# Kernel optimization log

Hardware: AMD Instinct MI355X
Metric: run time of the kernel (lower is better)

The kernel has to match this reference:

```python
import jax, jax.numpy as jnp
import numpy as np

B, IN, OUT = 8192, 256, 256

def setup_inputs() -> dict:
    key = jax.random.key(0)
    k1, k2 = jax.random.split(key)
    x = jax.random.normal(k1, (B, IN), dtype=jnp.float32)
    # kaiming_uniform_(a=sqrt(5)) -> U(-bound, bound), bound = sqrt(6/((1+a^2)*fan_in)) = sqrt(1/fan_in)
    bound = 1.0 / np.sqrt(IN + 1)
    weight = jax.random.uniform(k2, (OUT, IN + 1), dtype=jnp.float32, minval=-bound, maxval=bound)
    return {"x": x, "weight": weight}

def reference(x, weight):
    # augment x with ones column (bias term): (B, IN+1)
    x_aug = jnp.concatenate([x, jnp.ones((x.shape[0], 1), dtype=x.dtype)], axis=1)
    # lrelu(x, k) = clamp(k * x, min=0) = relu(weight * x) broadcast over (B, OUT, IN+1)
    y = jnp.maximum(weight[None, :, :] * x_aug[:, None, :], 0.0)
    return jnp.sum(y, axis=2)  # (B, OUT)
```

## Files before the change

### kernel.cpp

```cpp
#include <hip/hip_runtime.h>
#include <hip/hip_bf16.h>
#include <cstdint>


typedef short short8 __attribute__((ext_vector_type(8)));
typedef float f32x4 __attribute__((ext_vector_type(4)));

#define IN_F 256
#define OUT_F 256
#define KC 512
#define BM 32
#define BN 64
#define BK 64
#define NSTEP (KC / BK)

static __device__ __forceinline__ short f2bf(float f) {
    return __builtin_bit_cast(short, static_cast<__bf16>(f));
}

__global__ __launch_bounds__(64) void prep_kernel(const float* __restrict__ w,
                                                  short* __restrict__ Wcat,
                                                  float* __restrict__ bias) {
    const int o = blockIdx.x;
    const int t = threadIdx.x;
    const float* wr = w + (size_t)o * 257;
    float v[4];
#pragma unroll
    for (int j = 0; j < 4; ++j) v[j] = wr[t * 4 + j];
    short8 c;
#pragma unroll
    for (int j = 0; j < 4; ++j) {
        float h = 0.5f * v[j];
        c[2 * j]     = f2bf(h);
        c[2 * j + 1] = f2bf(__builtin_fabsf(h));
    }
    *reinterpret_cast<short8*>(Wcat + (size_t)o * KC + t * 8) = c;
    if (t == 0) bias[o] = __builtin_fmaxf(wr[256], 0.0f);
}

__global__ __launch_bounds__(256, 4) void skan_gemm(const float* __restrict__ x,
                                                    const short* __restrict__ Wcat,
                                                    const float* __restrict__ bias,
                                                    float* __restrict__ out) {
    __shared__ short Asm[2][BM][BK];
    __shared__ short Bsm[2][BN][BK];

    const int tid  = threadIdx.x;
    const int lane = tid & 63;
    const int wid  = tid >> 6;
    const int wr   = wid >> 1;
    const int wc   = wid & 1;
    const int m0   = blockIdx.x * BM;
    const int n0   = blockIdx.y * BN;

    const int ar = tid >> 3, ac = tid & 7;
    const float* aptr = x + (size_t)(m0 + ar) * IN_F + ac * 4;
    char* abase = (char*)&Asm[0][0][0];
    const int a_off = ar * 128 + ((ac ^ (ar & 7)) << 4);

    const int br = tid >> 2, bseg = tid & 3;
    const short* bptr = Wcat + (size_t)(n0 + br) * KC + bseg * 16;
    char* bbase = (char*)&Bsm[0][0][0];
    const int b_off0 = br * 128 + (((bseg * 2)     ^ (br & 7)) << 4);
    const int b_off1 = br * 128 + (((bseg * 2 + 1) ^ (br & 7)) << 4);

    f32x4 acc[2] = {};
    float4 areg;
    short8 breg0, breg1;

    auto loadRegs = [&](int kk) {
        areg  = *reinterpret_cast<const float4*>(aptr + kk * 32);
        breg0 = *reinterpret_cast<const short8*>(bptr + kk * BK);
        breg1 = *reinterpret_cast<const short8*>(bptr + kk * BK + 8);
    };
    auto writeLds = [&](int buf) {
        short8 av;
        const float vv[4] = {areg.x, areg.y, areg.z, areg.w};
#pragma unroll
        for (int j = 0; j < 4; ++j) {
            av[2 * j]     = f2bf(vv[j]);
            av[2 * j + 1] = f2bf(__builtin_fabsf(vv[j]));
        }
        *reinterpret_cast<short8*>(abase + buf * (BM * BK * 2) + a_off)  = av;
        *reinterpret_cast<short8*>(bbase + buf * (BN * BK * 2) + b_off0) = breg0;
        *reinterpret_cast<short8*>(bbase + buf * (BN * BK * 2) + b_off1) = breg1;
    };
    auto compute = [&](int buf) {
        const char* ab = abase + buf * (BM * BK * 2);
        const char* bb = bbase + buf * (BN * BK * 2);
        const int arow  = wr * 16 + (lane & 15);
        const int bcol0 = wc * 32 + (lane & 15);
        const int kg    = lane >> 4;
#pragma unroll
        for (int ks = 0; ks < 2; ++ks) {
            const int chunk = ks * 4 + kg;
            short8 af = *reinterpret_cast<const short8*>(
                ab + arow * 128 + ((chunk ^ (arow & 7)) << 4));
#pragma unroll
            for (int f = 0; f < 2; ++f) {
                const int bcol = bcol0 + f * 16;
                short8 bfr = *reinterpret_cast<const short8*>(
                    bb + bcol * 128 + ((chunk ^ (bcol & 7)) << 4));
                acc[f] = __builtin_amdgcn_mfma_f32_16x16x32_bf16(af, bfr, acc[f], 0, 0, 0);
            }
        }
    };

    loadRegs(0);
    writeLds(0);
    __syncthreads();
    int buf = 0;
#pragma unroll
    for (int kk = 0; kk < NSTEP; ++kk) {
        if (kk < NSTEP - 1) loadRegs(kk + 1);
        compute(buf);
        if (kk < NSTEP - 1) writeLds(buf ^ 1);
        __syncthreads();
        buf ^= 1;
    }

    const int col_l = lane & 15;
    const int rgrp  = lane >> 4;
#pragma unroll
    for (int f = 0; f < 2; ++f) {
        const int col = n0 + wc * 32 + f * 16 + col_l;
        const float bv = bias[col];
#pragma unroll
        for (int r = 0; r < 4; ++r) {
            const int row = m0 + wr * 16 + rgrp * 4 + r;
            out[(size_t)row * OUT_F + col] = acc[f][r] + bv;
        }
    }
}

extern "C" void kernel_launch(void* const* d_in, const int* in_sizes, int n_in,
                              void* d_out, int out_size, void* d_ws, size_t ws_size,
                              hipStream_t stream) {
    const float* x = (const float*)d_in[0];
    const float* w = (const float*)d_in[1];
    float* out = (float*)d_out;

    short* Wcat = (short*)d_ws;
    float* bias = (float*)((char*)d_ws + (size_t)OUT_F * KC * 2);

    prep_kernel<<<dim3(OUT_F), dim3(64), 0, stream>>>(w, Wcat, bias);
    skan_gemm<<<dim3(8192 / BM, OUT_F / BN), dim3(256), 0, stream>>>(x, Wcat, bias, out);
}
```

Before: 66.94 us.

## Pre-swizzle weights into MFMA fragment order and drop LDS staging

The weight-prep kernel now writes weights directly in 32x32x16 MFMA B-fragment order. The GEMM kernel reads A straight from global memory into registers, converts it to bf16 pairs there, and issues 32x32x16 MFMAs with two independent accumulators. This removes shared memory, the double-buffer pipeline and the __syncthreads barriers. The bias is read straight from the weight row instead of a precomputed buffer. The cost is that each wave reads x directly from global with no reuse across waves, and the grid has fewer, larger blocks (64 rows by 64 columns, 512 blocks).

```diff
diff --git a/kernel.cpp b/kernel.cpp
--- a/kernel.cpp
+++ b/kernel.cpp
@@ -4,132 +4,77 @@
 
 
 typedef short short8 __attribute__((ext_vector_type(8)));
-typedef float f32x4 __attribute__((ext_vector_type(4)));
+typedef float f32x4  __attribute__((ext_vector_type(4)));
+typedef float f32x16 __attribute__((ext_vector_type(16)));
 
-#define IN_F 256
-#define OUT_F 256
-#define KC 512
-#define BM 32
-#define BN 64
-#define BK 64
-#define NSTEP (KC / BK)
+#define NKK 32
 
 static __device__ __forceinline__ short f2bf(float f) {
     return __builtin_bit_cast(short, static_cast<__bf16>(f));
 }
 
-__global__ __launch_bounds__(64) void prep_kernel(const float* __restrict__ w,
-                                                  short* __restrict__ Wcat,
-                                                  float* __restrict__ bias) {
-    const int o = blockIdx.x;
-    const int t = threadIdx.x;
-    const float* wr = w + (size_t)o * 257;
-    float v[4];
+__global__ __launch_bounds__(64) void prep_wfrag(const float* __restrict__ w,
+                                                 short* __restrict__ Wfrag) {
+    const int nblk = blockIdx.x;
+    const int kk   = blockIdx.y;
+    const int lane = threadIdx.x;
+    const int col  = nblk * 32 + (lane & 31);
+    const int c0   = kk * 8 + (lane >> 5) * 4;
+    const float* wr = w + (size_t)col * 257 + c0;
+    short8 v;
 #pragma unroll
-    for (int j = 0; j < 4; ++j) v[j] = wr[t * 4 + j];
-    short8 c;
-#pragma unroll
-    for (int j = 0; j < 4; ++j) {
-        float h = 0.5f * v[j];
-        c[2 * j]     = f2bf(h);
-        c[2 * j + 1] = f2bf(__builtin_fabsf(h));
+    for (int t = 0; t < 4; ++t) {
+        const float h = 0.5f * wr[t];
+        v[2 * t]     = f2bf(h);
+        v[2 * t + 1] = f2bf(__builtin_fabsf(h));
     }
-    *reinterpret_cast<short8*>(Wcat + (size_t)o * KC + t * 8) = c;
-    if (t == 0) bias[o] = __builtin_fmaxf(wr[256], 0.0f);
+    *reinterpret_cast<short8*>(Wfrag + ((size_t)(nblk * 32 + kk) * 64 + lane) * 8) = v;
 }
 
-__global__ __launch_bounds__(256, 4) void skan_gemm(const float* __restrict__ x,
-                                                    const short* __restrict__ Wcat,
-                                                    const float* __restrict__ bias,
-                                                    float* __restrict__ out) {
-    __shared__ short Asm[2][BM][BK];
-    __shared__ short Bsm[2][BN][BK];
+__global__ __launch_bounds__(256) void skan_gemm(const float* __restrict__ x,
+                                                 const short* __restrict__ Wfrag,
+                                                 const float* __restrict__ w,
+                                                 float* __restrict__ out) {
+    const int tid   = threadIdx.x;
+    const int lane  = tid & 63;
+    const int wid   = tid >> 6;
+    const int wm    = wid & 1;
+    const int wn    = wid >> 1;
+    const int m0    = blockIdx.x * 64 + wm * 32;
+    const int nf    = blockIdx.y * 2 + wn;
+    const int rlane = lane & 31;
+    const int khalf = lane >> 5;
 
-    const int tid  = threadIdx.x;
-    const int lane = tid & 63;
-    const int wid  = tid >> 6;
-    const int wr   = wid >> 1;
-    const int wc   = wid & 1;
-    const int m0   = blockIdx.x * BM;
-    const int n0   = blockIdx.y * BN;
+    const float* xp = x + (size_t)(m0 + rlane) * 256 + khalf * 4;
+    const short* bp = Wfrag + ((size_t)nf * NKK * 64 + lane) * 8;
 
-    const int ar = tid >> 3, ac = tid & 7;
-    const float* aptr = x + (size_t)(m0 + ar) * IN_F + ac * 4;
-    char* abase = (char*)&Asm[0][0][0];
-    const int a_off = ar * 128 + ((ac ^ (ar & 7)) << 4);
+    f32x16 acc0 = {}, acc1 = {};
+#pragma unroll 4
+    for (int kk = 0; kk < NKK; kk += 2) {
+        const f32x4 v0 = *reinterpret_cast<const f32x4*>(xp + (size_t)kk * 8);
+        const short8 b0 = *reinterpret_cast<const short8*>(bp + (size_t)kk * 512);
+        const f32x4 v1 = *reinterpret_cast<const f32x4*>(xp + (size_t)(kk + 1) * 8);
+        const short8 b1 = *reinterpret_cast<const short8*>(bp + (size_t)(kk + 1) * 512);
+        short8 a0, a1;
+#pragma unroll
+        for (int t = 0; t < 4; ++t) {
+            a0[2 * t]     = f2bf(v0[t]);
+            a0[2 * t + 1] = f2bf(__builtin_fabsf(v0[t]));
+            a1[2 * t]     = f2bf(v1[t]);
+            a1[2 * t + 1] = f2bf(__builtin_fabsf(v1[t]));
+        }
+        acc0 = __builtin_amdgcn_mfma_f32_32x32x16_bf16(a0, b0, acc0, 0, 0, 0);
+        acc1 = __builtin_amdgcn_mfma_f32_32x32x16_bf16(a1, b1, acc1, 0, 0, 0);
+    }
+    const f32x16 acc = acc0 + acc1;
 
-    const int br = tid >> 2, bseg = tid & 3;
-    const short* bptr = Wcat + (size_t)(n0 + br) * KC + bseg * 16;
-    char* bbase = (char*)&Bsm[0][0][0];
-    const int b_off0 = br * 128 + (((bseg * 2)     ^ (br & 7)) << 4);
-    const int b_off1 = br * 128 + (((bseg * 2 + 1) ^ (br & 7)) << 4);
-
-    f32x4 acc[2] = {};
-    float4 areg;
-    short8 breg0, breg1;
-
-    auto loadRegs = [&](int kk) {
-        areg  = *reinterpret_cast<const float4*>(aptr + kk * 32);
-        breg0 = *reinterpret_cast<const short8*>(bptr + kk * BK);
-        breg1 = *reinterpret_cast<const short8*>(bptr + kk * BK + 8);
-    };
-    auto writeLds = [&](int buf) {
-        short8 av;
-        const float vv[4] = {areg.x, areg.y, areg.z, areg.w};
+    const int col  = nf * 32 + rlane;
+    const float bias = __builtin_fmaxf(w[(size_t)col * 257 + 256], 0.0f);
+    float* op = out + (size_t)(m0 + khalf * 4) * 256 + col;
 #pragma unroll
-        for (int j = 0; j < 4; ++j) {
-            av[2 * j]     = f2bf(vv[j]);
-            av[2 * j + 1] = f2bf(__builtin_fabsf(vv[j]));
-        }
-        *reinterpret_cast<short8*>(abase + buf * (BM * BK * 2) + a_off)  = av;
-        *reinterpret_cast<short8*>(bbase + buf * (BN * BK * 2) + b_off0) = breg0;
-        *reinterpret_cast<short8*>(bbase + buf * (BN * BK * 2) + b_off1) = breg1;
-    };
-    auto compute = [&](int buf) {
-        const char* ab = abase + buf * (BM * BK * 2);
-        const char* bb = bbase + buf * (BN * BK * 2);
-        const int arow  = wr * 16 + (lane & 15);
-        const int bcol0 = wc * 32 + (lane & 15);
-        const int kg    = lane >> 4;
-#pragma unroll
-        for (int ks = 0; ks < 2; ++ks) {
-            const int chunk = ks * 4 + kg;
-            short8 af = *reinterpret_cast<const short8*>(
-                ab + arow * 128 + ((chunk ^ (arow & 7)) << 4));
-#pragma unroll
-            for (int f = 0; f < 2; ++f) {
-                const int bcol = bcol0 + f * 16;
-                short8 bfr = *reinterpret_cast<const short8*>(
-                    bb + bcol * 128 + ((chunk ^ (bcol & 7)) << 4));
-                acc[f] = __builtin_amdgcn_mfma_f32_16x16x32_bf16(af, bfr, acc[f], 0, 0, 0);
-            }
-        }
-    };
-
-    loadRegs(0);
-    writeLds(0);
-    __syncthreads();
-    int buf = 0;
-#pragma unroll
-    for (int kk = 0; kk < NSTEP; ++kk) {
-        if (kk < NSTEP - 1) loadRegs(kk + 1);
-        compute(buf);
-        if (kk < NSTEP - 1) writeLds(buf ^ 1);
-        __syncthreads();
-        buf ^= 1;
-    }
-
-    const int col_l = lane & 15;
-    const int rgrp  = lane >> 4;
-#pragma unroll
-    for (int f = 0; f < 2; ++f) {
-        const int col = n0 + wc * 32 + f * 16 + col_l;
-        const float bv = bias[col];
-#pragma unroll
-        for (int r = 0; r < 4; ++r) {
-            const int row = m0 + wr * 16 + rgrp * 4 + r;
-            out[(size_t)row * OUT_F + col] = acc[f][r] + bv;
-        }
+    for (int r = 0; r < 16; ++r) {
+        const int orow = (r & 3) + 8 * (r >> 2);
+        op[(size_t)orow * 256] = acc[r] + bias;
     }
 }
 
@@ -140,9 +85,8 @@
     const float* w = (const float*)d_in[1];
     float* out = (float*)d_out;
 
-    short* Wcat = (short*)d_ws;
-    float* bias = (float*)((char*)d_ws + (size_t)OUT_F * KC * 2);
+    short* Wfrag = (short*)d_ws;
 
-    prep_kernel<<<dim3(OUT_F), dim3(64), 0, stream>>>(w, Wcat, bias);
-    skan_gemm<<<dim3(8192 / BM, OUT_F / BN), dim3(256), 0, stream>>>(x, Wcat, bias, out);
+    prep_wfrag<<<dim3(8, 32), dim3(64), 0, stream>>>(w, Wfrag);
+    skan_gemm<<<dim3(128, 4), dim3(256), 0, stream>>>(x, Wfrag, w, out);
 }
```

Result: slower. 70.88 us (+5.9%).
